# Kernel tuning notes

Hardware: AMD Instinct MI355X
Metric: run time of the kernel (lower is better)

## Reference

```python
import jax, jax.numpy as jnp
import numpy as np

NEG_SLOPE = 0.1   # LeakyReLU slope
EPS = 1e-5        # GroupNorm eps
GROUPS = 8        # out_feat // 16 = 128 // 16
NSAMPLE = 16      # naggre (k in KNN)
FEAT = 128        # feat_dim


def leaky(x):
    return jnp.where(x >= 0, x, NEG_SLOPE * x)


def gnorm(x, gamma, beta):
    # GroupNorm over channel dim 1; works for [B,C,N] and [B,C,N,K]
    B, C = x.shape[0], x.shape[1]
    sh = x.shape
    xg = x.reshape(B, GROUPS, -1)
    m = xg.mean(-1, keepdims=True)
    v = xg.var(-1, keepdims=True)
    xg = (xg - m) * jax.lax.rsqrt(v + EPS)
    br = (1, C) + (1,) * (len(sh) - 2)
    return xg.reshape(sh) * gamma.reshape(br) + beta.reshape(br)


def conv1(x, W, b):  # 1x1 Conv1d: x [B,C,N]
    return jnp.einsum('oc,bcn->bon', W, x) + b[None, :, None]


def conv2(x, W, b):  # 1x1 Conv2d: x [B,C,N,K]
    return jnp.einsum('oc,bcnk->bonk', W, x) + b[None, :, None, None]


def knn_idx(xyz, k):
    # xyz [B,3,N] -> idx [B,N,k] of k nearest points (self included)
    pts = xyz.transpose(0, 2, 1)                      # [B,N,3]
    sq = jnp.sum(pts * pts, axis=-1)                  # [B,N]
    d2 = sq[:, :, None] + sq[:, None, :] - 2.0 * jnp.einsum('bnc,bmc->bnm', pts, pts)
    _, idx = jax.lax.top_k(-d2, k)
    return idx


# grouping_operation: feat [B,C,N], idx [B,N,K] -> [B,C,N,K]
group = jax.vmap(lambda f, i: f[:, i])


def setup_inputs() -> dict:
    key = jax.random.key(0)
    ks = jax.random.split(key, 32)
    s = 0.05
    d = {
        'xyz': jax.random.normal(ks[0], (2, 3, 8192), jnp.float32),
        'feat': jax.random.normal(ks[1], (2, FEAT, 8192), jnp.float32),
        'W_pre': jax.random.normal(ks[2], (FEAT, FEAT), jnp.float32) * s,
        'b_pre': jnp.zeros((FEAT,), jnp.float32),
        'W_pos1': jax.random.normal(ks[3], (FEAT, 3), jnp.float32) * s,
        'b_pos1': jnp.zeros((FEAT,), jnp.float32),
        'g_pos1': jnp.ones((FEAT,), jnp.float32),
        'be_pos1': jnp.zeros((FEAT,), jnp.float32),
        'W_pos2': jax.random.normal(ks[4], (FEAT, FEAT), jnp.float32) * s,
        'b_pos2': jnp.zeros((FEAT,), jnp.float32),
        'W_q': jax.random.normal(ks[5], (FEAT, FEAT), jnp.float32) * s,
        'b_q': jnp.zeros((FEAT,), jnp.float32),
        'W_k': jax.random.normal(ks[6], (FEAT, FEAT), jnp.float32) * s,
        'b_k': jnp.zeros((FEAT,), jnp.float32),
        'W_v': jax.random.normal(ks[7], (FEAT, FEAT), jnp.float32) * s,
        'b_v': jnp.zeros((FEAT,), jnp.float32),
        'W_att1': jax.random.normal(ks[8], (FEAT, FEAT), jnp.float32) * s,
        'b_att1': jnp.zeros((FEAT,), jnp.float32),
        'g_att1': jnp.ones((FEAT,), jnp.float32),
        'be_att1': jnp.zeros((FEAT,), jnp.float32),
        'W_att2': jax.random.normal(ks[9], (FEAT, FEAT), jnp.float32) * s,
        'b_att2': jnp.zeros((FEAT,), jnp.float32),
        'W_post': jax.random.normal(ks[10], (FEAT, FEAT), jnp.float32) * s,
        'b_post': jnp.zeros((FEAT,), jnp.float32),
        'g_post': jnp.ones((FEAT,), jnp.float32),
        'be_post': jnp.zeros((FEAT,), jnp.float32),
    }
    return d


def reference(xyz, feat, W_pre, b_pre, W_pos1, b_pos1, g_pos1, be_pos1,
              W_pos2, b_pos2, W_q, b_q, W_k, b_k, W_v, b_v,
              W_att1, b_att1, g_att1, be_att1, W_att2, b_att2,
              W_post, b_post, g_post, be_post):
    idx = knn_idx(xyz, NSAMPLE)                       # [B,N,K]
    new_feat = conv1(feat, W_pre, b_pre)              # [B,C,N]
    rel = group(xyz, idx) - xyz[:, :, :, None]        # [B,3,N,K]
    pos = conv2(rel, W_pos1, b_pos1)
    pos = leaky(gnorm(pos, g_pos1, be_pos1))
    pos = conv2(pos, W_pos2, b_pos2)                  # [B,C,N,K]
    q = conv1(new_feat, W_q, b_q)
    k = group(conv1(new_feat, W_k, b_k), idx)
    v = group(conv1(new_feat, W_v, b_v), idx)
    att = q[:, :, :, None] - k + pos
    att = conv2(att, W_att1, b_att1)
    att = leaky(gnorm(att, g_att1, be_att1))
    att = conv2(att, W_att2, b_att2)
    att = jax.nn.softmax(att, axis=3)                 # softmax over neighbors
    out = jnp.sum(att * v, axis=3) + new_feat         # [B,C,N]
    out = leaky(gnorm(conv1(out, W_post, b_post), g_post, be_post))
    return out
```

## Files before the change

### kernel.cpp

```cpp
#include <hip/hip_runtime.h>
#include <hip/hip_bf16.h>
#include <float.h>

#define B_ 2
#define N_ 8192
#define C_ 128
#define K_ 16
#define G_ 8
#define NK_ (N_*K_)
#define BN_ (B_*N_)
#define BNK_ (B_*NK_)
#define CN_ (C_*N_)
#define NEG 0.1f
#define EPSV 1e-5f

typedef __attribute__((ext_vector_type(4))) float f32x4;
typedef __attribute__((ext_vector_type(8))) short s16x8;
typedef __attribute__((ext_vector_type(4))) short s16x4;

__device__ __forceinline__ float leakyf(float x){ return x >= 0.f ? x : NEG*x; }
__device__ __forceinline__ short f2b(float x){
  union { __hip_bfloat16 b; short s; } u; u.b = __float2bfloat16(x); return u.s;
}
__device__ __forceinline__ float b2f(short s){
  union { __hip_bfloat16 b; short s; } u; u.s = s; return __bfloat162float(u.b);
}

__device__ __forceinline__ int dpp_shr1_i(int x){
  return __builtin_amdgcn_update_dpp(x, x, 0x111, 0xF, 0xF, false);
}
__device__ __forceinline__ double dpp_shr1_d(double x){
  union { double d; int i[2]; } u; u.d = x;
  u.i[0] = dpp_shr1_i(u.i[0]);
  u.i[1] = dpp_shr1_i(u.i[1]);
  return u.d;
}
__device__ __forceinline__ double readlane_d(double x, int l){
  union { double d; int i[2]; } u; u.d = x;
  union { double d; int i[2]; } r;
  r.i[0] = __builtin_amdgcn_readlane(u.i[0], l);
  r.i[1] = __builtin_amdgcn_readlane(u.i[1], l);
  return r.d;
}

__global__ __launch_bounds__(256) void pack_kernel(const float* __restrict__ xyz, float4* __restrict__ pt4){
  int e = blockIdx.x*256 + threadIdx.x;
  int b = e >> 13, n = e & (N_-1);
  const float* xb = xyz + b*3*N_;
  float x = xb[n], y = xb[N_+n], z = xb[2*N_+n];
  pt4[e] = make_float4(x, y, z, x*x + y*y + z*z);
}

#define KNN_TPB 512
#define KNN_CHUNK 2048
#define KNN_MARGIN 2e-4f
__global__ __launch_bounds__(KNN_TPB) void knn_kernel(const float4* __restrict__ pt4, int* __restrict__ idxo){
  __shared__ float4 sp[KNN_CHUNK];
  int lane = threadIdx.x & 63, wid = threadIdx.x >> 6;
  int qg = blockIdx.x*(KNN_TPB/64) + wid;
  int b = qg >> 13, n = qg & (N_-1);
  const float4* pts = pt4 + b*N_;
  float4 qp = pts[n];
  double qx = qp.x, qy = qp.y, qz = qp.z;
  double qsq = qx*qx + qy*qy + qz*qz;
  float qx2 = -2.f*qp.x, qy2 = -2.f*qp.y, qz2 = -2.f*qp.z;
  double myd; int myi;
  float cmpv;

  {
    float4 pp = pts[lane];
    double px = pp.x, py = pp.y, pz = pp.z;
    double psq = px*px + py*py + pz*pz;
    double dot = qx*px + qy*py + qz*pz;
    double d2l = qsq + psq - 2.0*dot;
    int il = lane;
    #pragma unroll
    for (int k2 = 2; k2 <= 64; k2 <<= 1){
      #pragma unroll
      for (int mm = k2>>1; mm > 0; mm >>= 1){
        double pd = __shfl_xor(d2l, mm, 64);
        int pi = __shfl_xor(il, mm, 64);
        bool up = ((lane & k2) == 0);
        bool lower = ((lane & mm) == 0);
        bool myLess = (d2l < pd) || (d2l == pd && il < pi);
        bool keep = lower ? (up ? myLess : !myLess) : (up ? !myLess : myLess);
        if (!keep){ d2l = pd; il = pi; }
      }
    }
    myd = d2l; myi = il;
    double thr0 = readlane_d(myd, 15);
    cmpv = (float)(thr0 - qsq) + KNN_MARGIN;
  }

  auto process = [&](unsigned long long m, double d2v, int base){
    while (m){
      int src = __ffsll(m) - 1; m &= m - 1;
      double dn = readlane_d(d2v, src);
      int in_ = base + src;
      bool less = (dn < myd) || (dn == myd && in_ < myi);
      unsigned long long bm = __ballot(less) & 0xFFFFull;
      if (bm){
        int pos = __ffsll(bm) - 1;
        double pd = dpp_shr1_d(myd);
        int pi = dpp_shr1_i(myi);
        if (lane < 16){
          if (lane > pos){ myd = pd; myi = pi; }
          else if (lane == pos){ myd = dn; myi = in_; }
        }
      }
    }
  };

  for (int c0 = 0; c0 < N_; c0 += KNN_CHUNK){
    __syncthreads();
    #pragma unroll
    for (int t = 0; t < KNN_CHUNK/KNN_TPB; t++){
      int i = t*KNN_TPB + threadIdx.x;
      sp[i] = pts[c0 + i];
    }
    __syncthreads();
    for (int j0 = 0; j0 < KNN_CHUNK; j0 += 128){
      float4 pA = sp[j0 + lane];
      float4 pB = sp[j0 + 64 + lane];
      float fA = fmaf(pA.x, qx2, fmaf(pA.y, qy2, fmaf(pA.z, qz2, pA.w)));
      float fB = fmaf(pB.x, qx2, fmaf(pB.y, qy2, fmaf(pB.z, qz2, pB.w)));
      unsigned long long mA = __ballot(fA < cmpv);
      unsigned long long mB = __ballot(fB < cmpv);
      if (c0 == 0 && j0 == 0) mA = 0;
      if (mA | mB){
        if (mA){
          double px = pA.x, py = pA.y, pz = pA.z;
          double psq = px*px + py*py + pz*pz;
          double dot = qx*px + qy*py + qz*pz;
          double d2 = qsq + psq - 2.0*dot;
          process(mA, d2, c0 + j0);
        }
        if (mB){
          double px = pB.x, py = pB.y, pz = pB.z;
          double psq = px*px + py*py + pz*pz;
          double dot = qx*px + qy*py + qz*pz;
          double d2 = qsq + psq - 2.0*dot;
          process(mB, d2, c0 + j0 + 64);
        }
        double thr = readlane_d(myd, 15);
        cmpv = (float)(thr - qsq) + KNN_MARGIN;
      }
    }
  }
  if (lane < 16) idxo[qg*K_ + lane] = myi;
}

__global__ __launch_bounds__(256) void featb_kernel(const float* __restrict__ feat, ushort* __restrict__ fb){
  int p = blockIdx.x*256 + threadIdx.x;
  int b = p >> 13, n = p & (N_-1);
  const float* xin = feat + b*CN_ + n;
  #pragma unroll
  for (int c0 = 0; c0 < C_; c0 += 8){
    s16x8 o8;
    #pragma unroll
    for (int i = 0; i < 8; i++) o8[i] = f2b(xin[(size_t)(c0+i)*N_]);
    *(s16x8*)(fb + (size_t)p*C_ + c0) = o8;
  }
}

__global__ __launch_bounds__(256) void setup_kernel(const float* __restrict__ W_att1,
    const float* __restrict__ W_pos2, const float* __restrict__ W_q, const float* __restrict__ W_k,
    const float* __restrict__ b_pos2, const float* __restrict__ b_att1,
    const float* __restrict__ b_q, const float* __restrict__ b_k,
    float* __restrict__ Wf, float* __restrict__ Wqa, float* __restrict__ Wka,
    float* __restrict__ bG1, float* __restrict__ bqa, float* __restrict__ bka){
  int bx = blockIdx.x;
  if (bx < 192){
    int which = bx >> 6;
    const float* Bm = which==0 ? W_pos2 : (which==1 ? W_q : W_k);
    float* Cm = which==0 ? Wf : (which==1 ? Wqa : Wka);
    int e = (bx & 63)*256 + threadIdx.x;
    int o = e >> 7, c = e & 127;
    float s = 0.f;
    #pragma unroll 8
    for (int m = 0; m < 128; m++) s += W_att1[o*128+m]*Bm[m*128+c];
    Cm[e] = s;
  } else {
    for (int t = threadIdx.x; t < 384; t += 256){
      int which = t >> 7, o = t & 127;
      const float* v = which==0 ? b_pos2 : (which==1 ? b_q : b_k);
      float* out = which==0 ? bG1 : (which==1 ? bqa : bka);
      float s = which==0 ? b_att1[o] : 0.f;
      for (int m = 0; m < 128; m++) s += W_att1[o*128+m]*v[m];
      out[o] = s;
    }
  }
}

__global__ __launch_bounds__(256) void pos_stats_kernel(const float4* __restrict__ pt4,
    const int* __restrict__ idx, const float* __restrict__ W1, const float* __restrict__ b1,
    float* __restrict__ gsum, float* __restrict__ gssq){
  __shared__ float ls[G_], lss[G_];
  if (threadIdx.x < G_){ ls[threadIdx.x] = 0.f; lss[threadIdx.x] = 0.f; }
  __syncthreads();
  int p = blockIdx.x*256 + threadIdx.x;
  int b = p >> 17;
  int n = p >> 4;
  int j = idx[p];
  float4 pj = pt4[(b<<13) + j], pn = pt4[n];
  float rx = pj.x - pn.x, ry = pj.y - pn.y, rz = pj.z - pn.z;
  #pragma unroll
  for (int g = 0; g < G_; g++){
    float s = 0.f, ss = 0.f;
    #pragma unroll
    for (int ci = 0; ci < 16; ci++){
      int c = g*16 + ci;
      float v = b1[c] + W1[3*c]*rx + W1[3*c+1]*ry + W1[3*c+2]*rz;
      s += v; ss += v*v;
    }
    #pragma unroll
    for (int mk = 32; mk; mk >>= 1){ s += __shfl_xor(s, mk, 64); ss += __shfl_xor(ss, mk, 64); }
    if ((threadIdx.x & 63) == 0){ atomicAdd(&ls[g], s); atomicAdd(&lss[g], ss); }
  }
  __syncthreads();
  if (threadIdx.x < G_){
    atomicAdd(&gsum[b*G_ + threadIdx.x], ls[threadIdx.x]);
    atomicAdd(&gssq[b*G_ + threadIdx.x], lss[threadIdx.x]);
  }
}

__global__ void posfin_kernel(const float* __restrict__ gsum, const float* __restrict__ gssq,
    const float* __restrict__ W1, const float* __restrict__ b1,
    const float* __restrict__ g1, const float* __restrict__ be1, float* __restrict__ prm, float invcnt){
  __shared__ float sm[16], sr[16];
  int i = threadIdx.x;
  if (i < 16){
    float m = gsum[i]*invcnt;
    float v = gssq[i]*invcnt - m*m;
    v = fmaxf(v, 0.f);
    sm[i] = m; sr[i] = rsqrtf(v + EPSV);
  }
  __syncthreads();
  int b = i >> 7, c = i & 127, g = c >> 4;
  float rs = sr[b*G_+g]*g1[c];
  prm[b*512 +   0 + c] = W1[3*c]*rs;
  prm[b*512 + 128 + c] = W1[3*c+1]*rs;
  prm[b*512 + 256 + c] = W1[3*c+2]*rs;
  prm[b*512 + 384 + c] = (b1[c]-sm[b*G_+g])*rs + be1[c];
}

__global__ void attfin_kernel(const float* __restrict__ gsum, const float* __restrict__ gssq,
    const float* __restrict__ ga, const float* __restrict__ bea, float* __restrict__ prm, float invcnt){
  __shared__ float sm[16], sr[16];
  int i = threadIdx.x;
  if (i < 16){
    float m = gsum[i]*invcnt;
    float v = gssq[i]*invcnt - m*m;
    v = fmaxf(v, 0.f);
    sm[i] = m; sr[i] = rsqrtf(v + EPSV);
  }
  __syncthreads();
  int b = i >> 7, c = i & 127, g = c >> 4;
  float sc = ga[c]*sr[b*G_+g];
  prm[b*256 +   0 + c] = sc;
  prm[b*256 + 128 + c] = bea[c] - sm[b*G_+g]*sc;
}

#define ST_COPY 0
#define ST_GN   1
#define ST_POS  2
#define EP_PM    0
#define EP_QKS   1
#define EP_F32CM 2

template<int STAGE>
__device__ __forceinline__ void stage_x(ushort* xs,
    const ushort* __restrict__ Xb, const float* __restrict__ prm,
    const float4* __restrict__ pt4, const int* __restrict__ idx, int p0, int b)
{
  int tid = threadIdx.x;
  int row = tid & 63, cc = tid >> 6;
  if constexpr (STAGE == ST_COPY){
    const ushort* src = Xb + (size_t)(p0+row)*C_ + cc*32;
    #pragma unroll
    for (int q = 0; q < 4; q++){
      s16x8 v8 = *(const s16x8*)(src + q*8);
      int sl = (cc*4+q) ^ (row&7);
      *(s16x8*)(xs + row*C_ + sl*8) = v8;
    }
  } else if constexpr (STAGE == ST_GN){
    const ushort* src = Xb + (size_t)(p0+row)*C_ + cc*32;
    const float* sc = prm + b*256;
    const float* sh = prm + b*256 + 128;
    #pragma unroll
    for (int q = 0; q < 4; q++){
      s16x8 v8 = *(const s16x8*)(src + q*8);
      s16x8 o8;
      #pragma unroll
      for (int i = 0; i < 8; i++){
        int c = cc*32 + q*8 + i;
        o8[i] = f2b(leakyf(b2f(v8[i])*sc[c] + sh[c]));
      }
      int sl = (cc*4+q) ^ (row&7);
      *(s16x8*)(xs + row*C_ + sl*8) = o8;
    }
  } else {
    int p = p0 + row;
    int ng = p >> 4;
    int j = idx[p];
    float4 pj = pt4[(b<<13) + j], pn = pt4[ng];
    float rx = pj.x - pn.x, ry = pj.y - pn.y, rz = pj.z - pn.z;
    const float* sx = prm + b*512;
    const float* sy = sx + 128;
    const float* sz = sx + 256;
    const float* so = sx + 384;
    #pragma unroll
    for (int q = 0; q < 4; q++){
      s16x8 o8;
      #pragma unroll
      for (int i = 0; i < 8; i++){
        int c = cc*32 + q*8 + i;
        o8[i] = f2b(leakyf(sx[c]*rx + sy[c]*ry + sz[c]*rz + so[c]));
      }
      int sl = (cc*4+q) ^ (row&7);
      *(s16x8*)(xs + row*C_ + sl*8) = o8;
    }
  }
}

__device__ __forceinline__ void load_afr(s16x8 afr[2][4], const float* __restrict__ W, int wid, int lm, int lh){
  #pragma unroll
  for (int t = 0; t < 2; t++){
    int T = wid*2 + t;
    #pragma unroll
    for (int ks = 0; ks < 4; ks++){
      const float* wr = W + (size_t)(T*16 + lm)*C_ + ks*32 + lh*8;
      float4 w0 = *(const float4*)wr;
      float4 w1 = *(const float4*)(wr+4);
      s16x8 a;
      a[0]=f2b(w0.x); a[1]=f2b(w0.y); a[2]=f2b(w0.z); a[3]=f2b(w0.w);
      a[4]=f2b(w1.x); a[5]=f2b(w1.y); a[6]=f2b(w1.z); a[7]=f2b(w1.w);
      afr[t][ks] = a;
    }
  }
}

__device__ __forceinline__ void mfma_tile(f32x4 acc[2][4], const s16x8 afr[2][4],
    const ushort* xs, const float* __restrict__ bias, int wid, int lm, int lh)
{
  #pragma unroll
  for (int t = 0; t < 2; t++){
    f32x4 bs = *(const f32x4*)(bias + (wid*2+t)*16 + lh*4);
    #pragma unroll
    for (int ps = 0; ps < 4; ps++) acc[t][ps] = bs;
  }
  #pragma unroll
  for (int ps = 0; ps < 4; ps++){
    int row = ps*16 + lm;
    s16x8 bf[4];
    #pragma unroll
    for (int ks = 0; ks < 4; ks++){
      int sl = (ks*4+lh) ^ (row&7);
      bf[ks] = *(const s16x8*)(xs + row*C_ + sl*8);
    }
    #pragma unroll
    for (int ks = 0; ks < 4; ks++){
      #pragma unroll
      for (int t = 0; t < 2; t++)
        acc[t][ps] = __builtin_amdgcn_mfma_f32_16x16x32_bf16(afr[t][ks], bf[ks], acc[t][ps], 0,0,0);
    }
  }
}

template<int STAGE, int EPI>
__device__ __forceinline__ void mgemm_body(ushort* xs, float* sblk,
    const ushort* __restrict__ Xb, const float* __restrict__ W, const float* __restrict__ bias,
    const float* __restrict__ prm, const float4* __restrict__ pt4, const int* __restrict__ idx,
    const ushort* __restrict__ Aq, const ushort* __restrict__ Ak,
    void* __restrict__ Y, float* __restrict__ gsum, float* __restrict__ gssq, int bsh, int bx)
{
  int tid = threadIdx.x;
  int l = tid & 63, wid = tid >> 6;
  int lm = l & 15, lh = l >> 4;
  int p0 = bx * 64;
  int b = p0 >> bsh;

  if (tid < 16) sblk[tid] = 0.f;

  s16x8 afr[2][4];
  load_afr(afr, W, wid, lm, lh);
  stage_x<STAGE>(xs, Xb, prm, pt4, idx, p0, b);
  __syncthreads();

  f32x4 acc[2][4];
  mfma_tile(acc, afr, xs, bias, wid, lm, lh);

  float gs[2] = {0.f,0.f}, gq[2] = {0.f,0.f};
  #pragma unroll
  for (int t = 0; t < 2; t++){
    int T = wid*2 + t;
    int o0 = T*16 + lh*4;
    #pragma unroll
    for (int ps = 0; ps < 4; ps++){
      int p = p0 + ps*16 + lm;
      if constexpr (EPI == EP_PM){
        s16x4 r4;
        #pragma unroll
        for (int r = 0; r < 4; r++) r4[r] = f2b(acc[t][ps][r]);
        *(s16x4*)((ushort*)Y + (size_t)p*C_ + o0) = r4;
      } else if constexpr (EPI == EP_QKS){
        int ng = p >> 4;
        int j = idx[p];
        s16x4 aq4 = *(const s16x4*)(Aq + (size_t)ng*C_ + o0);
        s16x4 ak4 = *(const s16x4*)(Ak + ((size_t)(b<<13)+j)*C_ + o0);
        s16x4 r4;
        #pragma unroll
        for (int r = 0; r < 4; r++){
          float v = acc[t][ps][r] + b2f(aq4[r]) - b2f(ak4[r]);
          r4[r] = f2b(v);
          gs[t] += v; gq[t] += v*v;
        }
        *(s16x4*)((ushort*)Y + (size_t)p*C_ + o0) = r4;
      } else {
        float* yf = (float*)Y;
        #pragma unroll
        for (int r = 0; r < 4; r++){
          float v = acc[t][ps][r];
          yf[(size_t)(o0+r)*BN_ + p] = v;
          gs[t] += v; gq[t] += v*v;
        }
      }
    }
  }

  if constexpr (EPI == EP_QKS || EPI == EP_F32CM){
    #pragma unroll
    for (int t = 0; t < 2; t++){
      float s = gs[t], q = gq[t];
      #pragma unroll
      for (int mk = 32; mk; mk >>= 1){ s += __shfl_xor(s, mk, 64); q += __shfl_xor(q, mk, 64); }
      if (l == 0){
        int T = wid*2 + t;
        atomicAdd(&sblk[T], s); atomicAdd(&sblk[8+T], q);
      }
    }
    __syncthreads();
    if (tid < 8){
      atomicAdd(&gsum[b*G_ + tid], sblk[tid]);
      atomicAdd(&gssq[b*G_ + tid], sblk[8+tid]);
    }
  }
}

template<int STAGE, int EPI>
__global__ __launch_bounds__(256) void mgemm_kernel(
    const ushort* __restrict__ Xb, const float* __restrict__ W, const float* __restrict__ bias,
    const float* __restrict__ prm, const float4* __restrict__ pt4, const int* __restrict__ idx,
    const ushort* __restrict__ Aq, const ushort* __restrict__ Ak,
    void* __restrict__ Y, float* __restrict__ gsum, float* __restrict__ gssq, int bsh)
{
  __shared__ ushort xs[64*128];
  __shared__ float sblk[16];
  mgemm_body<STAGE,EPI>(xs, sblk, Xb, W, bias, prm, pt4, idx, Aq, Ak, Y, gsum, gssq, bsh, blockIdx.x);
}

__global__ __launch_bounds__(256) void qkv_kernel(const ushort* __restrict__ nfb,
    const float* __restrict__ Wv, const float* __restrict__ bv,
    const float* __restrict__ Wqa, const float* __restrict__ bqa,
    const float* __restrict__ Wka, const float* __restrict__ bka,
    ushort* __restrict__ vb, ushort* __restrict__ Aqb, ushort* __restrict__ Akb)
{
  __shared__ ushort xs[64*128];
  __shared__ float sblk[16];
  if (blockIdx.y == 0)
    mgemm_body<ST_COPY,EP_PM>(xs, sblk, nfb, Wv, bv, nullptr, nullptr, nullptr, nullptr, nullptr, vb, nullptr, nullptr, 13, blockIdx.x);
  else if (blockIdx.y == 1)
    mgemm_body<ST_COPY,EP_PM>(xs, sblk, nfb, Wqa, bqa, nullptr, nullptr, nullptr, nullptr, nullptr, Aqb, nullptr, nullptr, 13, blockIdx.x);
  else
    mgemm_body<ST_COPY,EP_PM>(xs, sblk, nfb, Wka, bka, nullptr, nullptr, nullptr, nullptr, nullptr, Akb, nullptr, nullptr, 13, blockIdx.x);
}

__global__ __launch_bounds__(256) void fatt_kernel(const ushort* __restrict__ Xb ,
    const float* __restrict__ W , const float* __restrict__ bias ,
    const float* __restrict__ prm , const int* __restrict__ idx,
    const ushort* __restrict__ vb, const ushort* __restrict__ nfb, ushort* __restrict__ outb)
{
  __shared__ ushort xs[64*128];
  int tid = threadIdx.x;
  int l = tid & 63, wid = tid >> 6;
  int lm = l & 15, lh = l >> 4;
  int p0 = blockIdx.x * 64;
  int b = p0 >> 17;

  s16x8 afr[2][4];
  load_afr(afr, W, wid, lm, lh);
  stage_x<ST_GN>(xs, Xb, prm, nullptr, nullptr, p0, b);
  __syncthreads();

  f32x4 acc[2][4];
  mfma_tile(acc, afr, xs, bias, wid, lm, lh);

  #pragma unroll
  for (int t = 0; t < 2; t++){
    int o0 = (wid*2+t)*16 + lh*4;
    #pragma unroll
    for (int ps = 0; ps < 4; ps++){
      int p = p0 + ps*16 + lm;
      int j = idx[p];
      s16x4 v4 = *(const s16x4*)(vb + ((size_t)(b<<13)+j)*C_ + o0);
      f32x4 e, pv;
      #pragma unroll
      for (int r = 0; r < 4; r++){
        float ev = __expf(acc[t][ps][r]);
        e[r] = ev;
        pv[r] = ev * b2f(v4[r]);
      }
      #pragma unroll
      for (int mk = 1; mk < 16; mk <<= 1){
        #pragma unroll
        for (int r = 0; r < 4; r++){
          e[r]  += __shfl_xor(e[r], mk, 64);
          pv[r] += __shfl_xor(pv[r], mk, 64);
        }
      }
      if (lm == 0){
        int n = p >> 4;
        s16x4 n4 = *(const s16x4*)(nfb + (size_t)n*C_ + o0);
        s16x4 o4;
        #pragma unroll
        for (int r = 0; r < 4; r++) o4[r] = f2b(pv[r]/e[r] + b2f(n4[r]));
        *(s16x4*)(outb + (size_t)n*C_ + o0) = o4;
      }
    }
  }
}

__global__ __launch_bounds__(256) void final_kernel(const float* __restrict__ out1,
    const float* __restrict__ gsum, const float* __restrict__ gssq,
    const float* __restrict__ g, const float* __restrict__ be, float* __restrict__ out){
  int e = blockIdx.x*256 + threadIdx.x;
  int b = e >> 20;
  int c = (e >> 13) & (C_-1);
  int n = e & (N_-1);
  int gi = b*G_ + (c >> 4);
  const float invcnt = 1.0f/(float)(16*N_);
  float m = gsum[gi]*invcnt;
  float var = gssq[gi]*invcnt - m*m;
  var = fmaxf(var, 0.f);
  float r = rsqrtf(var + EPSV);
  float v = (out1[(size_t)c*BN_ + b*N_ + n] - m) * r;
  v = v*g[c] + be[c];
  out[e] = leakyf(v);
}

extern "C" void kernel_launch(void* const* d_in, const int* in_sizes, int n_in,
                              void* d_out, int out_size, void* d_ws, size_t ws_size,
                              hipStream_t stream) {
  const float* xyz    = (const float*)d_in[0];
  const float* feat   = (const float*)d_in[1];
  const float* W_pre  = (const float*)d_in[2];
  const float* b_pre  = (const float*)d_in[3];
  const float* W_pos1 = (const float*)d_in[4];
  const float* b_pos1 = (const float*)d_in[5];
  const float* g_pos1 = (const float*)d_in[6];
  const float* be_pos1= (const float*)d_in[7];
  const float* W_pos2 = (const float*)d_in[8];
  const float* b_pos2 = (const float*)d_in[9];
  const float* W_q    = (const float*)d_in[10];
  const float* b_q    = (const float*)d_in[11];
  const float* W_k    = (const float*)d_in[12];
  const float* b_k    = (const float*)d_in[13];
  const float* W_v    = (const float*)d_in[14];
  const float* b_v    = (const float*)d_in[15];
  const float* W_att1 = (const float*)d_in[16];
  const float* b_att1 = (const float*)d_in[17];
  const float* g_att1 = (const float*)d_in[18];
  const float* be_att1= (const float*)d_in[19];
  const float* W_att2 = (const float*)d_in[20];
  const float* b_att2 = (const float*)d_in[21];
  const float* W_post = (const float*)d_in[22];
  const float* b_post = (const float*)d_in[23];
  const float* g_post = (const float*)d_in[24];
  const float* be_post= (const float*)d_in[25];

  char* w = (char*)d_ws;
  float4* pt4 = (float4*)w;            w += sizeof(float4)*BN_;
  int* idx = (int*)w;                  w += sizeof(int)*BNK_;
  ushort* fb   = (ushort*)w;           w += (size_t)2*BN_*C_;
  ushort* nfb  = (ushort*)w;           w += (size_t)2*BN_*C_;
  ushort* vb   = (ushort*)w;           w += (size_t)2*BN_*C_;
  ushort* Aqb  = (ushort*)w;           w += (size_t)2*BN_*C_;
  ushort* Akb  = (ushort*)w;           w += (size_t)2*BN_*C_;
  ushort* outb = (ushort*)w;           w += (size_t)2*BN_*C_;
  float* out1  = (float*)w;            w += (size_t)4*BN_*C_;
  ushort* bufA = (ushort*)w;           w += (size_t)2*BNK_*C_;
  float* Wf    = (float*)w;            w += sizeof(float)*C_*C_;
  float* Wqa   = (float*)w;            w += sizeof(float)*C_*C_;
  float* Wka   = (float*)w;            w += sizeof(float)*C_*C_;
  float* bG1   = (float*)w;            w += 512;
  float* bqa   = (float*)w;            w += 512;
  float* bka   = (float*)w;            w += 512;
  float* posPrm= (float*)w;            w += sizeof(float)*1024;
  float* attPrm= (float*)w;            w += sizeof(float)*512;
  float* stats = (float*)w;            w += 1024;

  float* pos_sum = stats +  0, *pos_ssq = stats + 16;
  float* att_sum = stats + 64, *att_ssq = stats + 80;
  float* post_sum= stats +128, *post_ssq= stats +144;

  hipMemsetAsync(stats, 0, 1024, stream);

  pack_kernel<<<BN_/256, 256, 0, stream>>>(xyz, pt4);
  knn_kernel<<<BN_/(KNN_TPB/64), KNN_TPB, 0, stream>>>(pt4, idx);
  featb_kernel<<<BN_/256, 256, 0, stream>>>(feat, fb);

  setup_kernel<<<193, 256, 0, stream>>>(W_att1, W_pos2, W_q, W_k, b_pos2, b_att1, b_q, b_k,
      Wf, Wqa, Wka, bG1, bqa, bka);

  mgemm_kernel<ST_COPY,EP_PM><<<BN_/64, 256, 0, stream>>>(fb, W_pre, b_pre, nullptr, nullptr, nullptr,
      nullptr, nullptr, nfb, nullptr, nullptr, 13);
  qkv_kernel<<<dim3(BN_/64, 3), 256, 0, stream>>>(nfb, W_v, b_v, Wqa, bqa, Wka, bka, vb, Aqb, Akb);

  pos_stats_kernel<<<BNK_/256, 256, 0, stream>>>(pt4, idx, W_pos1, b_pos1, pos_sum, pos_ssq);
  posfin_kernel<<<1, 256, 0, stream>>>(pos_sum, pos_ssq, W_pos1, b_pos1, g_pos1, be_pos1, posPrm,
      1.0f/(float)(16.0*NK_));

  mgemm_kernel<ST_POS,EP_QKS><<<BNK_/64, 256, 0, stream>>>(nullptr, Wf, bG1, posPrm, pt4, idx,
      Aqb, Akb, bufA, att_sum, att_ssq, 17);
  attfin_kernel<<<1, 256, 0, stream>>>(att_sum, att_ssq, g_att1, be_att1, attPrm, 1.0f/(float)(16.0*NK_));

  fatt_kernel<<<BNK_/64, 256, 0, stream>>>(bufA, W_att2, b_att2, attPrm, idx, vb, nfb, outb);

  mgemm_kernel<ST_COPY,EP_F32CM><<<BN_/64, 256, 0, stream>>>(outb, W_post, b_post, nullptr, nullptr, nullptr,
      nullptr, nullptr, out1, post_sum, post_ssq, 13);
  final_kernel<<<(B_*CN_)/256, 256, 0, stream>>>(out1, post_sum, post_ssq, g_post, be_post, (float*)d_out);
}
```

Before: 368.4 us.

## Pack KNN distance and index into sortable 64-bit keys, fuse pack kernels

Encodes each candidate's double distance with its 13-bit point index in the low mantissa bits, so the KNN sort and insertion compare and shuffle a single 64-bit key instead of a double plus an int. Merges the xyz pack and feature bf16 transpose into one kernel to drop a launch. Also interleaves the GroupNorm parameter arrays into float4/float2 records so each channel needs one vector load. Truncating the mantissa can change tie-breaking among nearly equidistant neighbors.

New measurement: 351.5 us. 4.6% less time.

```diff
diff --git a/kernel.cpp b/kernel.cpp
--- a/kernel.cpp
+++ b/kernel.cpp
@@ -29,26 +29,44 @@
 __device__ __forceinline__ int dpp_shr1_i(int x){
   return __builtin_amdgcn_update_dpp(x, x, 0x111, 0xF, 0xF, false);
 }
-__device__ __forceinline__ double dpp_shr1_d(double x){
-  union { double d; int i[2]; } u; u.d = x;
+__device__ __forceinline__ unsigned long long dpp_shr1_u64(unsigned long long x){
+  union { unsigned long long q; int i[2]; } u; u.q = x;
   u.i[0] = dpp_shr1_i(u.i[0]);
   u.i[1] = dpp_shr1_i(u.i[1]);
-  return u.d;
-}
-__device__ __forceinline__ double readlane_d(double x, int l){
-  union { double d; int i[2]; } u; u.d = x;
-  union { double d; int i[2]; } r;
+  return u.q;
+}
+__device__ __forceinline__ unsigned long long readlane_u64(unsigned long long x, int l){
+  union { unsigned long long q; int i[2]; } u; u.q = x;
+  union { unsigned long long q; int i[2]; } r;
   r.i[0] = __builtin_amdgcn_readlane(u.i[0], l);
   r.i[1] = __builtin_amdgcn_readlane(u.i[1], l);
-  return r.d;
-}
-
-__global__ __launch_bounds__(256) void pack_kernel(const float* __restrict__ xyz, float4* __restrict__ pt4){
+  return r.q;
+}
+__device__ __forceinline__ unsigned long long d2key(double d2, int idx){
+  d2 = fmax(d2, 0.0);
+  union { double d; unsigned long long q; } u; u.d = d2;
+  return (u.q & ~0x1FFFull) | (unsigned long long)idx;
+}
+__device__ __forceinline__ double key_upper_d2(unsigned long long k){
+  union { unsigned long long q; double d; } u; u.q = k | 0x1FFFull;
+  return u.d;
+}
+
+__global__ __launch_bounds__(256) void pack_featb_kernel(const float* __restrict__ xyz,
+    const float* __restrict__ feat, float4* __restrict__ pt4, ushort* __restrict__ fb){
   int e = blockIdx.x*256 + threadIdx.x;
   int b = e >> 13, n = e & (N_-1);
   const float* xb = xyz + b*3*N_;
   float x = xb[n], y = xb[N_+n], z = xb[2*N_+n];
   pt4[e] = make_float4(x, y, z, x*x + y*y + z*z);
+  const float* xin = feat + b*CN_ + n;
+  #pragma unroll
+  for (int c0 = 0; c0 < C_; c0 += 8){
+    s16x8 o8;
+    #pragma unroll
+    for (int i = 0; i < 8; i++) o8[i] = f2b(xin[(size_t)(c0+i)*N_]);
+    *(s16x8*)(fb + (size_t)e*C_ + c0) = o8;
+  }
 }
 
 #define KNN_TPB 512
@@ -64,7 +82,7 @@
   double qx = qp.x, qy = qp.y, qz = qp.z;
   double qsq = qx*qx + qy*qy + qz*qz;
   float qx2 = -2.f*qp.x, qy2 = -2.f*qp.y, qz2 = -2.f*qp.z;
-  double myd; int myi;
+  unsigned long long mykey;
   float cmpv;
 
   {
@@ -72,40 +90,35 @@
     double px = pp.x, py = pp.y, pz = pp.z;
     double psq = px*px + py*py + pz*pz;
     double dot = qx*px + qy*py + qz*pz;
-    double d2l = qsq + psq - 2.0*dot;
-    int il = lane;
+    unsigned long long kl = d2key(qsq + psq - 2.0*dot, lane);
     #pragma unroll
     for (int k2 = 2; k2 <= 64; k2 <<= 1){
       #pragma unroll
       for (int mm = k2>>1; mm > 0; mm >>= 1){
-        double pd = __shfl_xor(d2l, mm, 64);
-        int pi = __shfl_xor(il, mm, 64);
+        unsigned long long pk = __shfl_xor(kl, mm, 64);
         bool up = ((lane & k2) == 0);
         bool lower = ((lane & mm) == 0);
-        bool myLess = (d2l < pd) || (d2l == pd && il < pi);
+        bool myLess = kl < pk;
         bool keep = lower ? (up ? myLess : !myLess) : (up ? !myLess : myLess);
-        if (!keep){ d2l = pd; il = pi; }
-      }
-    }
-    myd = d2l; myi = il;
-    double thr0 = readlane_d(myd, 15);
-    cmpv = (float)(thr0 - qsq) + KNN_MARGIN;
-  }
-
-  auto process = [&](unsigned long long m, double d2v, int base){
+        if (!keep) kl = pk;
+      }
+    }
+    mykey = kl;
+    cmpv = (float)(key_upper_d2(readlane_u64(mykey, 15)) - qsq) + KNN_MARGIN;
+  }
+
+  auto process = [&](unsigned long long m, unsigned long long keyv){
     while (m){
       int src = __ffsll(m) - 1; m &= m - 1;
-      double dn = readlane_d(d2v, src);
-      int in_ = base + src;
-      bool less = (dn < myd) || (dn == myd && in_ < myi);
+      unsigned long long kn = readlane_u64(keyv, src);
+      bool less = kn < mykey;
       unsigned long long bm = __ballot(less) & 0xFFFFull;
       if (bm){
         int pos = __ffsll(bm) - 1;
-        double pd = dpp_shr1_d(myd);
-        int pi = dpp_shr1_i(myi);
+        unsigned long long pk = dpp_shr1_u64(mykey);
         if (lane < 16){
-          if (lane > pos){ myd = pd; myi = pi; }
-          else if (lane == pos){ myd = dn; myi = in_; }
+          if (lane > pos) mykey = pk;
+          else if (lane == pos) mykey = kn;
         }
       }
     }
@@ -132,35 +145,19 @@
           double px = pA.x, py = pA.y, pz = pA.z;
           double psq = px*px + py*py + pz*pz;
           double dot = qx*px + qy*py + qz*pz;
-          double d2 = qsq + psq - 2.0*dot;
-          process(mA, d2, c0 + j0);
+          process(mA, d2key(qsq + psq - 2.0*dot, c0 + j0 + lane));
         }
         if (mB){
           double px = pB.x, py = pB.y, pz = pB.z;
           double psq = px*px + py*py + pz*pz;
           double dot = qx*px + qy*py + qz*pz;
-          double d2 = qsq + psq - 2.0*dot;
-          process(mB, d2, c0 + j0 + 64);
+          process(mB, d2key(qsq + psq - 2.0*dot, c0 + j0 + 64 + lane));
         }
-        double thr = readlane_d(myd, 15);
-        cmpv = (float)(thr - qsq) + KNN_MARGIN;
-      }
-    }
-  }
-  if (lane < 16) idxo[qg*K_ + lane] = myi;
-}
-
-__global__ __launch_bounds__(256) void featb_kernel(const float* __restrict__ feat, ushort* __restrict__ fb){
-  int p = blockIdx.x*256 + threadIdx.x;
-  int b = p >> 13, n = p & (N_-1);
-  const float* xin = feat + b*CN_ + n;
-  #pragma unroll
-  for (int c0 = 0; c0 < C_; c0 += 8){
-    s16x8 o8;
-    #pragma unroll
-    for (int i = 0; i < 8; i++) o8[i] = f2b(xin[(size_t)(c0+i)*N_]);
-    *(s16x8*)(fb + (size_t)p*C_ + c0) = o8;
-  }
+        cmpv = (float)(key_upper_d2(readlane_u64(mykey, 15)) - qsq) + KNN_MARGIN;
+      }
+    }
+  }
+  if (lane < 16) idxo[qg*K_ + lane] = (int)(mykey & 0x1FFFull);
 }
 
 __global__ __launch_bounds__(256) void setup_kernel(const float* __restrict__ W_att1,
@@ -238,10 +235,9 @@
   __syncthreads();
   int b = i >> 7, c = i & 127, g = c >> 4;
   float rs = sr[b*G_+g]*g1[c];
-  prm[b*512 +   0 + c] = W1[3*c]*rs;
-  prm[b*512 + 128 + c] = W1[3*c+1]*rs;
-  prm[b*512 + 256 + c] = W1[3*c+2]*rs;
-  prm[b*512 + 384 + c] = (b1[c]-sm[b*G_+g])*rs + be1[c];
+  float4* p4 = (float4*)prm;
+  p4[b*128 + c] = make_float4(W1[3*c]*rs, W1[3*c+1]*rs, W1[3*c+2]*rs,
+                              (b1[c]-sm[b*G_+g])*rs + be1[c]);
 }
 
 __global__ void attfin_kernel(const float* __restrict__ gsum, const float* __restrict__ gssq,
@@ -257,8 +253,8 @@
   __syncthreads();
   int b = i >> 7, c = i & 127, g = c >> 4;
   float sc = ga[c]*sr[b*G_+g];
-  prm[b*256 +   0 + c] = sc;
-  prm[b*256 + 128 + c] = bea[c] - sm[b*G_+g]*sc;
+  float2* p2 = (float2*)prm;
+  p2[b*128 + c] = make_float2(sc, bea[c] - sm[b*G_+g]*sc);
 }
 
 #define ST_COPY 0
@@ -285,8 +281,7 @@
     }
   } else if constexpr (STAGE == ST_GN){
     const ushort* src = Xb + (size_t)(p0+row)*C_ + cc*32;
-    const float* sc = prm + b*256;
-    const float* sh = prm + b*256 + 128;
+    const float2* pr = (const float2*)prm + b*128;
     #pragma unroll
     for (int q = 0; q < 4; q++){
       s16x8 v8 = *(const s16x8*)(src + q*8);
@@ -294,7 +289,8 @@
       #pragma unroll
       for (int i = 0; i < 8; i++){
         int c = cc*32 + q*8 + i;
-        o8[i] = f2b(leakyf(b2f(v8[i])*sc[c] + sh[c]));
+        float2 s2 = pr[c];
+        o8[i] = f2b(leakyf(b2f(v8[i])*s2.x + s2.y));
       }
       int sl = (cc*4+q) ^ (row&7);
       *(s16x8*)(xs + row*C_ + sl*8) = o8;
@@ -305,17 +301,15 @@
     int j = idx[p];
     float4 pj = pt4[(b<<13) + j], pn = pt4[ng];
     float rx = pj.x - pn.x, ry = pj.y - pn.y, rz = pj.z - pn.z;
-    const float* sx = prm + b*512;
-    const float* sy = sx + 128;
-    const float* sz = sx + 256;
-    const float* so = sx + 384;
+    const float4* pr = (const float4*)prm + b*128;
     #pragma unroll
     for (int q = 0; q < 4; q++){
       s16x8 o8;
       #pragma unroll
       for (int i = 0; i < 8; i++){
         int c = cc*32 + q*8 + i;
-        o8[i] = f2b(leakyf(sx[c]*rx + sy[c]*ry + sz[c]*rz + so[c]));
+        float4 s4 = pr[c];
+        o8[i] = f2b(leakyf(fmaf(s4.x, rx, fmaf(s4.y, ry, fmaf(s4.z, rz, s4.w)))));
       }
       int sl = (cc*4+q) ^ (row&7);
       *(s16x8*)(xs + row*C_ + sl*8) = o8;
@@ -605,9 +599,8 @@
 
   hipMemsetAsync(stats, 0, 1024, stream);
 
-  pack_kernel<<<BN_/256, 256, 0, stream>>>(xyz, pt4);
+  pack_featb_kernel<<<BN_/256, 256, 0, stream>>>(xyz, feat, pt4, fb);
   knn_kernel<<<BN_/(KNN_TPB/64), KNN_TPB, 0, stream>>>(pt4, idx);
-  featb_kernel<<<BN_/256, 256, 0, stream>>>(feat, fb);
 
   setup_kernel<<<193, 256, 0, stream>>>(W_att1, W_pos2, W_q, W_k, b_pos2, b_att1, b_q, b_k,
       Wf, Wqa, Wka, bG1, bqa, bka);
```
